# Kernel tuning notes

Hardware: AMD Instinct MI355X
Metric: run time of the kernel (lower is better)

The kernel has to match this reference:

```python
import jax, jax.numpy as jnp
import numpy as np

Z = 10        # number of negative samples per item
LAMB = 0.01   # L2 regularization weight


def setup_inputs() -> dict:
    key = jax.random.key(0)
    k = jax.random.split(key, 7)
    WE, DE, V, D, B, NG = 300, 256, 50000, 100000, 4096, 10
    return {
        "rv": jax.random.normal(k[0], (WE, V), dtype=jnp.float32),      # word embedding table (frozen in original)
        "rd": jax.random.normal(k[1], (DE, D), dtype=jnp.float32),      # document embedding table
        "proj": jax.random.normal(k[2], (DE, WE), dtype=jnp.float32) * (1.0 / np.sqrt(WE)),
        "beta": jax.random.uniform(k[3], (DE,), dtype=jnp.float32),
        "word_ids": jax.random.randint(k[4], (B, NG), 0, V),
        "doc_ids": jax.random.randint(k[5], (B,), 0, D),
        "neg_ids": jax.random.randint(k[6], (B, Z), 0, D),
    }


def reference(rv, rd, proj, beta, word_ids, doc_ids, neg_ids):
    # g: mean of n-gram word embeddings per sample -> (we, B)
    g = rv[:, word_ids].mean(axis=2)
    # norm: per-sample L2 normalization
    normed = g / jnp.linalg.norm(g, axis=0, keepdims=True)
    # f: project into document space -> (de, B)
    t_pre = proj @ normed
    # standardize across the batch (torch .std is unbiased, ddof=1);
    # NOTE: original divides by sqrt(std), faithfully reproduced
    mean = t_pre.mean(axis=1, keepdims=True)
    std = jnp.std(t_pre, axis=1, ddof=1, keepdims=True)
    t = jnp.clip((t_pre - mean) / jnp.sqrt(std) + beta[:, None], -1.0, 1.0)  # hardtanh
    # positive documents: (de, B)
    doc_emb = rd[:, doc_ids]
    p_pos = jnp.clip(jax.nn.sigmoid(jnp.sum(t * doc_emb, axis=0)), -0.999, 0.999)
    log_p = Z * jnp.log(p_pos)  # (B,)
    # negative samples: (de, B, Z)
    neg_emb = rd[:, neg_ids]
    p_neg = jnp.clip(jax.nn.sigmoid(jnp.einsum('db,dbz->bz', t, neg_emb)), -0.999, 0.999)
    nsample_log = jnp.sum(jnp.log(jnp.clip(1.0 - p_neg, 0.01, None)), axis=1)  # (B,)
    log_p_wave = (Z + 1) / (2 * Z) * (log_p + nsample_log)
    B = log_p_wave.shape[0]
    loss = jnp.sum(log_p_wave) / B + LAMB / (2 * B) * (jnp.sum(rd * rd) + jnp.sum(proj * proj))
    return loss
```

## Files before the change

kernel.cpp:

```cpp
#include <hip/hip_runtime.h>
#include <math.h>

#define WE 300
#define DEp 256
#define VV 50000
#define DDim 100000
#define BB 4096
#define NGc 10
#define RVT_STRIDE 304

__device__ __forceinline__ float wave_reduce(float v) {
    #pragma unroll
    for (int o = 32; o > 0; o >>= 1) v += __shfl_down(v, o, 64);
    return v;
}

__device__ __forceinline__ float wave_allreduce(float v) {
    #pragma unroll
    for (int o = 32; o > 0; o >>= 1) v += __shfl_xor(v, o, 64);
    return v;
}

__device__ __forceinline__ float logsigf(float x) {
    return (x >= 0.f) ? -log1pf(expf(-x)) : x - log1pf(expf(x));
}

__global__ void k_init(double* p, int n) {
    int i = blockIdx.x * blockDim.x + threadIdx.x;
    if (i < n) p[i] = 0.0;
}

__global__ __launch_bounds__(256) void k_trd(const float* __restrict__ in,
                                             float* __restrict__ out,
                                             double* __restrict__ reg_acc) {
    __shared__ float4 tile[32 * 64];
    const int N = DDim;
    int n0 = blockIdx.x * 32;
    int t = threadIdx.x;
    float ss = 0.f;
    #pragma unroll
    for (int i = 0; i < 2; ++i) {
        int flat = i * 256 + t;
        int qn = flat & 7;
        int qm = flat >> 3;
        int n = n0 + qn * 4;
        const float* p = in + (size_t)(qm * 4) * N + n;
        float4 v0 = *(const float4*)(p);
        float4 v1 = *(const float4*)(p + N);
        float4 v2 = *(const float4*)(p + 2 * (size_t)N);
        float4 v3 = *(const float4*)(p + 3 * (size_t)N);
        ss += v0.x * v0.x + v0.y * v0.y + v0.z * v0.z + v0.w * v0.w;
        ss += v1.x * v1.x + v1.y * v1.y + v1.z * v1.z + v1.w * v1.w;
        ss += v2.x * v2.x + v2.y * v2.y + v2.z * v2.z + v2.w * v2.w;
        ss += v3.x * v3.x + v3.y * v3.y + v3.z * v3.z + v3.w * v3.w;
        int r0 = qn * 4;
        tile[(r0 + 0) * 64 + (qm ^ (r0 + 0))] = make_float4(v0.x, v1.x, v2.x, v3.x);
        tile[(r0 + 1) * 64 + (qm ^ (r0 + 1))] = make_float4(v0.y, v1.y, v2.y, v3.y);
        tile[(r0 + 2) * 64 + (qm ^ (r0 + 2))] = make_float4(v0.z, v1.z, v2.z, v3.z);
        tile[(r0 + 3) * 64 + (qm ^ (r0 + 3))] = make_float4(v0.w, v1.w, v2.w, v3.w);
    }
    __syncthreads();
    size_t base = (size_t)n0 * DEp;
    #pragma unroll
    for (int i = 0; i < 8; ++i) {
        int j = i * 256 + t;
        int nl = j >> 6;
        int m4 = j & 63;
        *(float4*)(out + base + (size_t)j * 4) = tile[nl * 64 + (m4 ^ nl)];
    }
    float r = wave_reduce(ss);
    __shared__ float part[4];
    int lane = t & 63, wv = t >> 6;
    if (lane == 0) part[wv] = r;
    __syncthreads();
    if (t == 0)
        atomicAdd(reg_acc, (double)(part[0] + part[1] + part[2] + part[3]));
}

__global__ __launch_bounds__(256) void k_trv(const float* __restrict__ in,
                                             float* __restrict__ out) {
    __shared__ float4 tile[32 * 80];
    const int N = VV;
    int n0 = blockIdx.x * 32;
    int t = threadIdx.x;
    #pragma unroll
    for (int i = 0; i < 3; ++i) {
        int flat = i * 256 + t;
        if (flat < 600) {
            int qn = flat & 7;
            int qm = flat >> 3;
            int n = n0 + qn * 4;
            float4 v0, v1, v2, v3;
            if (n < N) {
                const float* p = in + (size_t)(qm * 4) * N + n;
                v0 = *(const float4*)(p);
                v1 = *(const float4*)(p + N);
                v2 = *(const float4*)(p + 2 * (size_t)N);
                v3 = *(const float4*)(p + 3 * (size_t)N);
            } else {
                v0 = v1 = v2 = v3 = make_float4(0.f, 0.f, 0.f, 0.f);
            }
            int r0 = qn * 4;
            tile[(r0 + 0) * 80 + (qm ^ ((r0 + 0) & 7))] = make_float4(v0.x, v1.x, v2.x, v3.x);
            tile[(r0 + 1) * 80 + (qm ^ ((r0 + 1) & 7))] = make_float4(v0.y, v1.y, v2.y, v3.y);
            tile[(r0 + 2) * 80 + (qm ^ ((r0 + 2) & 7))] = make_float4(v0.z, v1.z, v2.z, v3.z);
            tile[(r0 + 3) * 80 + (qm ^ ((r0 + 3) & 7))] = make_float4(v0.w, v1.w, v2.w, v3.w);
        }
    }
    __syncthreads();
    size_t base = (size_t)n0 * (RVT_STRIDE / 4);
    float4* out4 = (float4*)out;
    for (int i = 0; i < 10; ++i) {
        int j = i * 256 + t;
        if (j < 2432) {
            int nl = j / 76;
            int m4 = j - nl * 76;
            if (n0 + nl < N)
                out4[base + j] = tile[nl * 80 + (m4 ^ (nl & 7))];
        }
    }
}


__global__ __launch_bounds__(256) void k_gather2(const float* __restrict__ rvT,
                                                 const int* __restrict__ wid,
                                                 float* __restrict__ normed) {
    int wv = threadIdx.x >> 6, lane = threadIdx.x & 63;
    int b = blockIdx.x * 4 + wv;
    int id = 0;
    if (lane < NGc) id = wid[b * NGc + lane];
    float4 a  = make_float4(0.f, 0.f, 0.f, 0.f);
    float4 a2 = make_float4(0.f, 0.f, 0.f, 0.f);
    #pragma unroll
    for (int ng = 0; ng < NGc; ++ng) {
        int rid = __shfl(id, ng, 64);
        const float* row = rvT + (size_t)rid * RVT_STRIDE;
        float4 v = *(const float4*)(row + lane * 4);
        a.x += v.x; a.y += v.y; a.z += v.z; a.w += v.w;
        if (lane < 11) {
            float4 w = *(const float4*)(row + 256 + lane * 4);
            a2.x += w.x; a2.y += w.y; a2.z += w.z; a2.w += w.w;
        }
    }
    a.x *= 0.1f; a.y *= 0.1f; a.z *= 0.1f; a.w *= 0.1f;
    a2.x *= 0.1f; a2.y *= 0.1f; a2.z *= 0.1f; a2.w *= 0.1f;
    float ss = a.x * a.x + a.y * a.y + a.z * a.z + a.w * a.w
             + a2.x * a2.x + a2.y * a2.y + a2.z * a2.z + a2.w * a2.w;
    float s = wave_allreduce(ss);
    float s_inv = 1.0f / sqrtf(s);
    float* orow = normed + (size_t)b * WE;
    *(float4*)(orow + lane * 4) =
        make_float4(a.x * s_inv, a.y * s_inv, a.z * s_inv, a.w * s_inv);
    if (lane < 11)
        *(float4*)(orow + 256 + lane * 4) =
            make_float4(a2.x * s_inv, a2.y * s_inv, a2.z * s_inv, a2.w * s_inv);
}

__global__ __launch_bounds__(256) void k_loss2(const float* __restrict__ tpre,
                                               const float* __restrict__ meanf,
                                               const float* __restrict__ scalef,
                                               const float* __restrict__ beta,
                                               const float* __restrict__ rdT,
                                               const int* __restrict__ doc_ids,
                                               const int* __restrict__ neg_ids,
                                               double* __restrict__ acc) {
    int wv = threadIdx.x >> 6, lane = threadIdx.x & 63;
    int b = blockIdx.x * 4 + wv;

    float4 t4  = *(const float4*)(tpre + (size_t)b * DEp + lane * 4);
    float4 m4  = *(const float4*)(meanf + lane * 4);
    float4 sc4 = *(const float4*)(scalef + lane * 4);
    float4 be4 = *(const float4*)(beta + lane * 4);
    float tv0 = fminf(1.f, fmaxf(-1.f, (t4.x - m4.x) * sc4.x + be4.x));
    float tv1 = fminf(1.f, fmaxf(-1.f, (t4.y - m4.y) * sc4.y + be4.y));
    float tv2 = fminf(1.f, fmaxf(-1.f, (t4.z - m4.z) * sc4.z + be4.z));
    float tv3 = fminf(1.f, fmaxf(-1.f, (t4.w - m4.w) * sc4.w + be4.w));

    int id = 0;
    if (lane == 0) id = doc_ids[b];
    else if (lane < 11) id = neg_ids[b * NGc + lane - 1];

    float xv = 0.f;
    #pragma unroll
    for (int j = 0; j < 11; ++j) {
        int rid = __shfl(id, j, 64);
        float4 r4 = *(const float4*)(rdT + (size_t)rid * DEp + lane * 4);
        float p = tv0 * r4.x + tv1 * r4.y + tv2 * r4.z + tv3 * r4.w;
        p = wave_allreduce(p);
        if (lane == j) xv = p;
    }
    float contrib = 0.f;
    if (lane == 0)      contrib = 10.f * fminf(logsigf(xv), -1.0005003e-3f);
    else if (lane < 11) contrib = fmaxf(logsigf(-xv), -4.6051702f);
    #pragma unroll
    for (int o = 8; o > 0; o >>= 1) contrib += __shfl_down(contrib, o, 16);

    __shared__ float bp[4];
    if (lane == 0) bp[wv] = contrib;
    __syncthreads();
    if (threadIdx.x == 0)
        atomicAdd(acc, (double)(0.55f * (bp[0] + bp[1] + bp[2] + bp[3])));
}


__global__ __launch_bounds__(320) void k_gather(const float* __restrict__ rv,
                                                const int* __restrict__ wid,
                                                float* __restrict__ normed) {
    int b = blockIdx.x;
    int tid = threadIdx.x;
    __shared__ int ids[NGc];
    __shared__ float wpart[5];
    __shared__ float s_inv;
    if (tid < NGc) ids[tid] = wid[b * NGc + tid];
    __syncthreads();
    float g = 0.f;
    if (tid < WE) {
        const float* row = rv + (size_t)tid * VV;
        #pragma unroll
        for (int ng = 0; ng < NGc; ++ng) g += row[ids[ng]];
        g *= 0.1f;
    }
    float r = wave_reduce(g * g);
    int lane = tid & 63, wv = tid >> 6;
    if (lane == 0) wpart[wv] = r;
    __syncthreads();
    if (tid == 0) {
        float s = wpart[0] + wpart[1] + wpart[2] + wpart[3] + wpart[4];
        s_inv = 1.0f / sqrtf(s);
    }
    __syncthreads();
    if (tid < WE) normed[(size_t)b * WE + tid] = g * s_inv;
}

__global__ __launch_bounds__(256) void k_loss(const float* __restrict__ tpre,
                                              const float* __restrict__ meanf,
                                              const float* __restrict__ scalef,
                                              const float* __restrict__ beta,
                                              const float* __restrict__ rd,
                                              const int* __restrict__ doc_ids,
                                              const int* __restrict__ neg_ids,
                                              double* __restrict__ acc) {
    int b = blockIdx.x;
    int de = threadIdx.x;
    float t = tpre[(size_t)b * DEp + de];
    float tv = (t - meanf[de]) * scalef[de] + beta[de];
    tv = fminf(1.f, fmaxf(-1.f, tv));
    const float* rdrow = rd + (size_t)de * DDim;
    __shared__ int ids[11];
    if (de == 0) ids[0] = doc_ids[b];
    if (de >= 1 && de < 11) ids[de] = neg_ids[b * NGc + de - 1];
    __syncthreads();
    float prod[11];
    #pragma unroll
    for (int j = 0; j < 11; ++j) prod[j] = tv * rdrow[ids[j]];
    __shared__ float part[11][4];
    int lane = de & 63, wv = de >> 6;
    #pragma unroll
    for (int j = 0; j < 11; ++j) {
        float r = wave_reduce(prod[j]);
        if (lane == 0) part[j][wv] = r;
    }
    __syncthreads();
    if (de == 0) {
        float x0 = part[0][0] + part[0][1] + part[0][2] + part[0][3];
        float total = 10.f * fminf(logsigf(x0), -1.0005003e-3f);
        #pragma unroll
        for (int j = 1; j < 11; ++j) {
            float xj = part[j][0] + part[j][1] + part[j][2] + part[j][3];
            total += fmaxf(logsigf(-xj), -4.6051702f);
        }
        atomicAdd(acc, (double)(0.55f * total));
    }
}


__global__ __launch_bounds__(256) void k_gemm(const float* __restrict__ proj,
                                              const float* __restrict__ normed,
                                              float* __restrict__ tpre) {
    __shared__ float As[64 * 33];
    __shared__ float Bs[64 * 33];
    int tid = threadIdx.x;
    int tx = tid & 15, ty = tid >> 4;
    int de0 = blockIdx.y * 64;
    int b0  = blockIdx.x * 64;
    float acc[4][4] = {};
    int f = tid & 7, r0 = tid >> 3;
    for (int kt = 0; kt < 10; ++kt) {
        int k0 = kt * 32;
        __syncthreads();
        for (int rr = r0; rr < 64; rr += 32) {
            int k = k0 + f * 4;
            float4 va = make_float4(0.f, 0.f, 0.f, 0.f);
            float4 vb = make_float4(0.f, 0.f, 0.f, 0.f);
            if (k + 3 < WE) {
                va = *(const float4*)(proj + (size_t)(de0 + rr) * WE + k);
                vb = *(const float4*)(normed + (size_t)(b0 + rr) * WE + k);
            }
            float* ap = &As[rr * 33 + f * 4];
            ap[0] = va.x; ap[1] = va.y; ap[2] = va.z; ap[3] = va.w;
            float* bp = &Bs[rr * 33 + f * 4];
            bp[0] = vb.x; bp[1] = vb.y; bp[2] = vb.z; bp[3] = vb.w;
        }
        __syncthreads();
        #pragma unroll
        for (int k = 0; k < 32; ++k) {
            float a[4], bv[4];
            #pragma unroll
            for (int i = 0; i < 4; ++i) a[i] = As[(tx * 4 + i) * 33 + k];
            #pragma unroll
            for (int j = 0; j < 4; ++j) bv[j] = Bs[(ty * 4 + j) * 33 + k];
            #pragma unroll
            for (int j = 0; j < 4; ++j)
                #pragma unroll
                for (int i = 0; i < 4; ++i) acc[j][i] += a[i] * bv[j];
        }
    }
    #pragma unroll
    for (int jb = 0; jb < 4; ++jb) {
        int b = b0 + ty * 4 + jb;
        float4 v = make_float4(acc[jb][0], acc[jb][1], acc[jb][2], acc[jb][3]);
        *(float4*)(tpre + (size_t)b * DEp + de0 + tx * 4) = v;
    }
}

__global__ __launch_bounds__(256) void k_stats1(const float* __restrict__ tpre,
                                                double* __restrict__ rowsum,
                                                double* __restrict__ rowsq) {
    int de = threadIdx.x;
    int c0 = blockIdx.x * 64;
    float s = 0.f, ss = 0.f;
    for (int i = 0; i < 64; ++i) {
        float v = tpre[(size_t)(c0 + i) * DEp + de];
        s += v; ss += v * v;
    }
    atomicAdd(&rowsum[de], (double)s);
    atomicAdd(&rowsq[de], (double)ss);
}

__global__ void k_stats2(const double* __restrict__ rowsum, const double* __restrict__ rowsq,
                         float* __restrict__ meanf, float* __restrict__ scalef) {
    int de = threadIdx.x;
    double s = rowsum[de], ss = rowsq[de];
    double mean = s / (double)BB;
    double var = (ss - s * s / (double)BB) / (double)(BB - 1);
    double stdv = sqrt(var);
    meanf[de]  = (float)mean;
    scalef[de] = (float)(1.0 / sqrt(stdv));
}

__global__ __launch_bounds__(256) void k_reg(const float4* __restrict__ p, int n4,
                                             double* __restrict__ acc) {
    int idx = blockIdx.x * blockDim.x + threadIdx.x;
    int stride = gridDim.x * blockDim.x;
    float s = 0.f;
    for (int i = idx; i < n4; i += stride) {
        float4 v = p[i];
        s += v.x * v.x + v.y * v.y + v.z * v.z + v.w * v.w;
    }
    float r = wave_reduce(s);
    __shared__ float part[4];
    int lane = threadIdx.x & 63, wv = threadIdx.x >> 6;
    if (lane == 0) part[wv] = r;
    __syncthreads();
    if (threadIdx.x == 0)
        atomicAdd(acc, (double)(part[0] + part[1] + part[2] + part[3]));
}

__global__ void k_final(const double* __restrict__ accs, float* __restrict__ out) {
    double loss = accs[0] / (double)BB + (0.01 / (2.0 * (double)BB)) * (accs[1] + accs[2]);
    out[0] = (float)loss;
}

extern "C" void kernel_launch(void* const* d_in, const int* in_sizes, int n_in,
                              void* d_out, int out_size, void* d_ws, size_t ws_size,
                              hipStream_t stream) {
    const float* rv   = (const float*)d_in[0];
    const float* rd   = (const float*)d_in[1];
    const float* proj = (const float*)d_in[2];
    const float* beta = (const float*)d_in[3];
    const int* wid    = (const int*)d_in[4];
    const int* doc    = (const int*)d_in[5];
    const int* neg    = (const int*)d_in[6];
    float* out = (float*)d_out;
    char* ws = (char*)d_ws;

    const size_t off_big    = 0;
    const size_t off_normed = 102400000;
    const size_t off_tpre   = off_normed + 4915200;
    const size_t off_small  = off_tpre + 4194304;
    const size_t need = off_small + 1024 + 1024 + 2048 + 2048 + 24;

    if (ws_size >= need) {
        float*  rvT    = (float*)(ws + off_big);
        float*  rdT    = (float*)(ws + off_big);
        float*  normed = (float*)(ws + off_normed);
        float*  tpre   = (float*)(ws + off_tpre);
        float*  meanf  = (float*)(ws + off_small);
        float*  scalef = (float*)(ws + off_small + 1024);
        double* rowsum = (double*)(ws + off_small + 2048);
        double* rowsq  = (double*)(ws + off_small + 4096);
        double* accs   = (double*)(ws + off_small + 6144);

        k_init<<<3, 256, 0, stream>>>(rowsum, 515);
        k_trv<<<1563, 256, 0, stream>>>(rv, rvT);
        k_gather2<<<BB / 4, 256, 0, stream>>>(rvT, wid, normed);
        k_gemm<<<dim3(64, 4), 256, 0, stream>>>(proj, normed, tpre);
        k_stats1<<<64, 256, 0, stream>>>(tpre, rowsum, rowsq);
        k_stats2<<<1, 256, 0, stream>>>(rowsum, rowsq, meanf, scalef);
        k_trd<<<3125, 256, 0, stream>>>(rd, rdT, accs + 1);
        k_loss2<<<BB / 4, 256, 0, stream>>>(tpre, meanf, scalef, beta, rdT, doc, neg, accs);
        k_reg<<<75, 256, 0, stream>>>((const float4*)proj, 19200, accs + 2);
        k_final<<<1, 1, 0, stream>>>(accs, out);
    } else {
        float*  normed = (float*)(ws);
        float*  tpre   = (float*)(ws + 4915200);
        float*  meanf  = (float*)(ws + 9109504);
        float*  scalef = (float*)(ws + 9110528);
        double* rowsum = (double*)(ws + 9111552);
        double* rowsq  = (double*)(ws + 9113600);
        double* accs   = (double*)(ws + 9115648);

        k_init<<<3, 256, 0, stream>>>(rowsum, 515);
        k_gather<<<BB, 320, 0, stream>>>(rv, wid, normed);
        k_gemm<<<dim3(64, 4), 256, 0, stream>>>(proj, normed, tpre);
        k_stats1<<<64, 256, 0, stream>>>(tpre, rowsum, rowsq);
        k_stats2<<<1, 256, 0, stream>>>(rowsum, rowsq, meanf, scalef);
        k_loss<<<BB, 256, 0, stream>>>(tpre, meanf, scalef, beta, rd, doc, neg, accs);
        k_reg<<<1024, 256, 0, stream>>>((const float4*)rd, 6400000, accs + 1);
        k_reg<<<75, 256, 0, stream>>>((const float4*)proj, 19200, accs + 2);
        k_final<<<1, 1, 0, stream>>>(accs, out);
    }
}
```

Measured before the change: 295.7 us.

## Rewrite transposes with wide row-contiguous tiles and fuse column stats into GEMM

The rd and rv transpose kernels now process 128 columns per block with full-row float4 reads across 64-row chunks, replacing the narrow 32-column tiles. The aim is longer contiguous global reads and fewer blocks. The per-feature sum and sum-of-squares are now accumulated in the GEMM epilogue through shared and global atomics, which removes the separate stats kernel and its re-read of tpre. The costs are more global double atomics from GEMM blocks and a padded shared tile that may bank-conflict on the column-wise reads.

```diff
diff --git a/kernel.cpp b/kernel.cpp
--- a/kernel.cpp
+++ b/kernel.cpp
@@ -25,51 +25,53 @@
     return (x >= 0.f) ? -log1pf(expf(-x)) : x - log1pf(expf(x));
 }
 
-__global__ void k_init(double* p, int n) {
+__global__ void k_init(unsigned* p, int n) {
     int i = blockIdx.x * blockDim.x + threadIdx.x;
-    if (i < n) p[i] = 0.0;
+    if (i < n) p[i] = 0u;
 }
 
 __global__ __launch_bounds__(256) void k_trd(const float* __restrict__ in,
                                              float* __restrict__ out,
                                              double* __restrict__ reg_acc) {
-    __shared__ float4 tile[32 * 64];
+    __shared__ float tile[64 * 132];
+    __shared__ float part[4];
     const int N = DDim;
-    int n0 = blockIdx.x * 32;
     int t = threadIdx.x;
+    int tile0 = blockIdx.x * 128;
     float ss = 0.f;
-    #pragma unroll
-    for (int i = 0; i < 2; ++i) {
-        int flat = i * 256 + t;
-        int qn = flat & 7;
-        int qm = flat >> 3;
-        int n = n0 + qn * 4;
-        const float* p = in + (size_t)(qm * 4) * N + n;
-        float4 v0 = *(const float4*)(p);
-        float4 v1 = *(const float4*)(p + N);
-        float4 v2 = *(const float4*)(p + 2 * (size_t)N);
-        float4 v3 = *(const float4*)(p + 3 * (size_t)N);
-        ss += v0.x * v0.x + v0.y * v0.y + v0.z * v0.z + v0.w * v0.w;
-        ss += v1.x * v1.x + v1.y * v1.y + v1.z * v1.z + v1.w * v1.w;
-        ss += v2.x * v2.x + v2.y * v2.y + v2.z * v2.z + v2.w * v2.w;
-        ss += v3.x * v3.x + v3.y * v3.y + v3.z * v3.z + v3.w * v3.w;
-        int r0 = qn * 4;
-        tile[(r0 + 0) * 64 + (qm ^ (r0 + 0))] = make_float4(v0.x, v1.x, v2.x, v3.x);
-        tile[(r0 + 1) * 64 + (qm ^ (r0 + 1))] = make_float4(v0.y, v1.y, v2.y, v3.y);
-        tile[(r0 + 2) * 64 + (qm ^ (r0 + 2))] = make_float4(v0.z, v1.z, v2.z, v3.z);
-        tile[(r0 + 3) * 64 + (qm ^ (r0 + 3))] = make_float4(v0.w, v1.w, v2.w, v3.w);
-    }
-    __syncthreads();
-    size_t base = (size_t)n0 * DEp;
-    #pragma unroll
-    for (int i = 0; i < 8; ++i) {
-        int j = i * 256 + t;
-        int nl = j >> 6;
-        int m4 = j & 63;
-        *(float4*)(out + base + (size_t)j * 4) = tile[nl * 64 + (m4 ^ nl)];
+    for (int c = 0; c < 4; ++c) {
+        int de0 = c * 64;
+        if (c) __syncthreads();
+        #pragma unroll
+        for (int i = 0; i < 2; ++i) {
+            int r = i * 32 + (t >> 3);
+            #pragma unroll
+            for (int e = 0; e < 4; ++e) {
+                int f4c = (t & 7) * 4 + e;
+                int col = tile0 + f4c * 4;
+                float4 v = make_float4(0.f, 0.f, 0.f, 0.f);
+                if (col < N)
+                    v = *(const float4*)(in + (size_t)(de0 + r) * N + col);
+                ss += v.x * v.x + v.y * v.y + v.z * v.z + v.w * v.w;
+                *(float4*)(&tile[r * 132 + f4c * 4]) = v;
+            }
+        }
+        __syncthreads();
+        #pragma unroll
+        for (int i = 0; i < 8; ++i) {
+            int j = i * 256 + t;
+            int n = j >> 4;
+            int k = j & 15;
+            if (tile0 + n < N) {
+                float4 v = make_float4(tile[(4 * k + 0) * 132 + n],
+                                       tile[(4 * k + 1) * 132 + n],
+                                       tile[(4 * k + 2) * 132 + n],
+                                       tile[(4 * k + 3) * 132 + n]);
+                *(float4*)(out + (size_t)(tile0 + n) * DEp + de0 + 4 * k) = v;
+            }
+        }
     }
     float r = wave_reduce(ss);
-    __shared__ float part[4];
     int lane = t & 63, wv = t >> 6;
     if (lane == 0) part[wv] = r;
     __syncthreads();
@@ -79,44 +81,56 @@
 
 __global__ __launch_bounds__(256) void k_trv(const float* __restrict__ in,
                                              float* __restrict__ out) {
-    __shared__ float4 tile[32 * 80];
+    __shared__ float tile[64 * 132];
     const int N = VV;
-    int n0 = blockIdx.x * 32;
     int t = threadIdx.x;
-    #pragma unroll
-    for (int i = 0; i < 3; ++i) {
-        int flat = i * 256 + t;
-        if (flat < 600) {
-            int qn = flat & 7;
-            int qm = flat >> 3;
-            int n = n0 + qn * 4;
-            float4 v0, v1, v2, v3;
-            if (n < N) {
-                const float* p = in + (size_t)(qm * 4) * N + n;
-                v0 = *(const float4*)(p);
-                v1 = *(const float4*)(p + N);
-                v2 = *(const float4*)(p + 2 * (size_t)N);
-                v3 = *(const float4*)(p + 3 * (size_t)N);
-            } else {
-                v0 = v1 = v2 = v3 = make_float4(0.f, 0.f, 0.f, 0.f);
-            }
-            int r0 = qn * 4;
-            tile[(r0 + 0) * 80 + (qm ^ ((r0 + 0) & 7))] = make_float4(v0.x, v1.x, v2.x, v3.x);
-            tile[(r0 + 1) * 80 + (qm ^ ((r0 + 1) & 7))] = make_float4(v0.y, v1.y, v2.y, v3.y);
-            tile[(r0 + 2) * 80 + (qm ^ ((r0 + 2) & 7))] = make_float4(v0.z, v1.z, v2.z, v3.z);
-            tile[(r0 + 3) * 80 + (qm ^ ((r0 + 3) & 7))] = make_float4(v0.w, v1.w, v2.w, v3.w);
-        }
-    }
-    __syncthreads();
-    size_t base = (size_t)n0 * (RVT_STRIDE / 4);
-    float4* out4 = (float4*)out;
-    for (int i = 0; i < 10; ++i) {
-        int j = i * 256 + t;
-        if (j < 2432) {
-            int nl = j / 76;
-            int m4 = j - nl * 76;
-            if (n0 + nl < N)
-                out4[base + j] = tile[nl * 80 + (m4 ^ (nl & 7))];
+    int tile0 = blockIdx.x * 128;
+    for (int c = 0; c < 5; ++c) {
+        int de0 = c * 64;
+        if (c) __syncthreads();
+        #pragma unroll
+        for (int i = 0; i < 2; ++i) {
+            int r = i * 32 + (t >> 3);
+            #pragma unroll
+            for (int e = 0; e < 4; ++e) {
+                int f4c = (t & 7) * 4 + e;
+                int col = tile0 + f4c * 4;
+                float4 v = make_float4(0.f, 0.f, 0.f, 0.f);
+                if (col < N && (de0 + r) < WE)
+                    v = *(const float4*)(in + (size_t)(de0 + r) * N + col);
+                *(float4*)(&tile[r * 132 + f4c * 4]) = v;
+            }
+        }
+        __syncthreads();
+        if (c < 4) {
+            #pragma unroll
+            for (int i = 0; i < 8; ++i) {
+                int j = i * 256 + t;
+                int n = j >> 4;
+                int k = j & 15;
+                if (tile0 + n < N) {
+                    float4 v = make_float4(tile[(4 * k + 0) * 132 + n],
+                                           tile[(4 * k + 1) * 132 + n],
+                                           tile[(4 * k + 2) * 132 + n],
+                                           tile[(4 * k + 3) * 132 + n]);
+                    *(float4*)(out + (size_t)(tile0 + n) * RVT_STRIDE + de0 + 4 * k) = v;
+                }
+            }
+        } else {
+            for (int i = 0; i < 6; ++i) {
+                int j = i * 256 + t;
+                if (j < 128 * 11) {
+                    int n = j / 11;
+                    int k = j - n * 11;
+                    if (tile0 + n < N) {
+                        float4 v = make_float4(tile[(4 * k + 0) * 132 + n],
+                                               tile[(4 * k + 1) * 132 + n],
+                                               tile[(4 * k + 2) * 132 + n],
+                                               tile[(4 * k + 3) * 132 + n]);
+                        *(float4*)(out + (size_t)(tile0 + n) * RVT_STRIDE + 256 + 4 * k) = v;
+                    }
+                }
+            }
         }
     }
 }
@@ -276,9 +290,13 @@
 
 __global__ __launch_bounds__(256) void k_gemm(const float* __restrict__ proj,
                                               const float* __restrict__ normed,
-                                              float* __restrict__ tpre) {
+                                              float* __restrict__ tpre,
+                                              double* __restrict__ rowsum,
+                                              double* __restrict__ rowsq) {
     __shared__ float As[64 * 33];
     __shared__ float Bs[64 * 33];
+    __shared__ float sSum[64];
+    __shared__ float sSq[64];
     int tid = threadIdx.x;
     int tx = tid & 15, ty = tid >> 4;
     int de0 = blockIdx.y * 64;
@@ -321,20 +339,24 @@
         float4 v = make_float4(acc[jb][0], acc[jb][1], acc[jb][2], acc[jb][3]);
         *(float4*)(tpre + (size_t)b * DEp + de0 + tx * 4) = v;
     }
-}
-
-__global__ __launch_bounds__(256) void k_stats1(const float* __restrict__ tpre,
-                                                double* __restrict__ rowsum,
-                                                double* __restrict__ rowsq) {
-    int de = threadIdx.x;
-    int c0 = blockIdx.x * 64;
-    float s = 0.f, ss = 0.f;
-    for (int i = 0; i < 64; ++i) {
-        float v = tpre[(size_t)(c0 + i) * DEp + de];
-        s += v; ss += v * v;
-    }
-    atomicAdd(&rowsum[de], (double)s);
-    atomicAdd(&rowsq[de], (double)ss);
+    if (tid < 64) { sSum[tid] = 0.f; sSq[tid] = 0.f; }
+    __syncthreads();
+    #pragma unroll
+    for (int i = 0; i < 4; ++i) {
+        float ls = 0.f, lq = 0.f;
+        #pragma unroll
+        for (int jb = 0; jb < 4; ++jb) {
+            float v = acc[jb][i];
+            ls += v; lq += v * v;
+        }
+        atomicAdd(&sSum[tx * 4 + i], ls);
+        atomicAdd(&sSq[tx * 4 + i], lq);
+    }
+    __syncthreads();
+    if (tid < 64) {
+        atomicAdd(&rowsum[de0 + tid], (double)sSum[tid]);
+        atomicAdd(&rowsq[de0 + tid], (double)sSq[tid]);
+    }
 }
 
 __global__ void k_stats2(const double* __restrict__ rowsum, const double* __restrict__ rowsq,
@@ -401,13 +423,12 @@
         double* rowsq  = (double*)(ws + off_small + 4096);
         double* accs   = (double*)(ws + off_small + 6144);
 
-        k_init<<<3, 256, 0, stream>>>(rowsum, 515);
-        k_trv<<<1563, 256, 0, stream>>>(rv, rvT);
+        k_init<<<5, 256, 0, stream>>>((unsigned*)(ws + off_small + 2048), 1030);
+        k_trv<<<391, 256, 0, stream>>>(rv, rvT);
         k_gather2<<<BB / 4, 256, 0, stream>>>(rvT, wid, normed);
-        k_gemm<<<dim3(64, 4), 256, 0, stream>>>(proj, normed, tpre);
-        k_stats1<<<64, 256, 0, stream>>>(tpre, rowsum, rowsq);
+        k_gemm<<<dim3(64, 4), 256, 0, stream>>>(proj, normed, tpre, rowsum, rowsq);
         k_stats2<<<1, 256, 0, stream>>>(rowsum, rowsq, meanf, scalef);
-        k_trd<<<3125, 256, 0, stream>>>(rd, rdT, accs + 1);
+        k_trd<<<782, 256, 0, stream>>>(rd, rdT, accs + 1);
         k_loss2<<<BB / 4, 256, 0, stream>>>(tpre, meanf, scalef, beta, rdT, doc, neg, accs);
         k_reg<<<75, 256, 0, stream>>>((const float4*)proj, 19200, accs + 2);
         k_final<<<1, 1, 0, stream>>>(accs, out);
@@ -420,10 +441,9 @@
         double* rowsq  = (double*)(ws + 9113600);
         double* accs   = (double*)(ws + 9115648);
 
-        k_init<<<3, 256, 0, stream>>>(rowsum, 515);
+        k_init<<<5, 256, 0, stream>>>((unsigned*)(ws + 9111552), 1030);
         k_gather<<<BB, 320, 0, stream>>>(rv, wid, normed);
-        k_gemm<<<dim3(64, 4), 256, 0, stream>>>(proj, normed, tpre);
-        k_stats1<<<64, 256, 0, stream>>>(tpre, rowsum, rowsq);
+        k_gemm<<<dim3(64, 4), 256, 0, stream>>>(proj, normed, tpre, rowsum, rowsq);
         k_stats2<<<1, 256, 0, stream>>>(rowsum, rowsq, meanf, scalef);
         k_loss<<<BB, 256, 0, stream>>>(tpre, meanf, scalef, beta, rd, doc, neg, accs);
         k_reg<<<1024, 256, 0, stream>>>((const float4*)rd, 6400000, accs + 1);
```

Result: slower. 315.1 us (+6.5%).
